# Kernel tuning notes

Hardware: AMD Instinct MI355X
Metric: run time of the kernel (lower is better)

The kernel has to match this reference:

```python
import math
import jax, jax.numpy as jnp
import numpy as np

N = 262144
DIMS_IN = 8
DIMS_C = 4
UNITS = 64
BINS = 10
N_PERMS = 3  # ceil(log2(8))
N_BLOCKS = 2 * N_PERMS
MIN_BW = 0.001
MIN_BH = 0.001
MIN_D = 0.001
EPS = 1e-6
LOG2 = float(np.log(2.0))


def build_masks():
    bits = np.array([[int(ch) for ch in np.binary_repr(i, N_PERMS)] for i in range(DIMS_IN)])
    bits = bits[:, ::-1].T  # (N_PERMS, DIMS_IN), LSB-first
    m = np.repeat(bits, 2, axis=0).astype(bool)  # repeat_interleave(2, dim=0)
    m[1::2] ^= True
    return m

MASKS = build_masks()  # (6, 8) bool, each row has 4 True


def rational_quadratic_spline(inputs, uw, uh, ud):
    # inputs: (N, D); uw/uh: (N, D, K); ud: (N, D, K+1). left=bottom=0, right=top=1.
    K = uw.shape[-1]
    widths = MIN_BW + (1.0 - MIN_BW * K) * jax.nn.softmax(uw, axis=-1)
    cw = jnp.cumsum(widths, axis=-1)
    cw = jnp.concatenate([jnp.zeros_like(cw[..., :1]), cw], axis=-1)
    cw = cw.at[..., -1].set(1.0)
    widths = cw[..., 1:] - cw[..., :-1]

    deriv = (MIN_D + jax.nn.softplus(ud)) / (MIN_D + LOG2)

    heights = MIN_BH + (1.0 - MIN_BH * K) * jax.nn.softmax(uh, axis=-1)
    ch = jnp.cumsum(heights, axis=-1)
    ch = jnp.concatenate([jnp.zeros_like(ch[..., :1]), ch], axis=-1)
    ch = ch.at[..., -1].set(1.0)
    heights = ch[..., 1:] - ch[..., :-1]

    # searchsorted on bin edges (forward uses cumwidths)
    locs = cw.at[..., -1].add(EPS)
    bin_idx = jnp.clip(jnp.sum(inputs[..., None] >= locs, axis=-1) - 1, 0, K - 1)
    g = lambda a: jnp.take_along_axis(a, bin_idx[..., None], axis=-1)[..., 0]

    in_cw = g(cw)
    in_bw = g(widths)
    in_ch = g(ch)
    delta = heights / widths
    in_delta = g(delta)
    in_d = g(deriv)
    in_dp1 = g(deriv[..., 1:])
    in_h = g(heights)

    theta = (inputs - in_cw) / in_bw
    tomt = theta * (1.0 - theta)
    numerator = in_h * (in_delta * theta ** 2 + in_d * tomt)
    denominator = in_delta + (in_d + in_dp1 - 2.0 * in_delta) * tomt
    outputs = in_ch + numerator / denominator
    deriv_num = in_delta ** 2 * (in_dp1 * theta ** 2 + 2.0 * in_delta * tomt + in_d * (1.0 - theta) ** 2)
    logabsdet = jnp.log(deriv_num) - 2.0 * jnp.log(denominator)
    return outputs, logabsdet


def unconstrained_rqs(inputs, uw, uh, ud):
    inside = jnp.all((inputs >= 0.0) & (inputs <= 1.0), axis=-1)  # (N,)
    x_in = jnp.clip(inputs, 0.0, 1.0)
    o, lad = rational_quadratic_spline(x_in, uw, uh, ud)
    outputs = jnp.where(inside[:, None], o, inputs)
    logabsdet = jnp.where(inside[:, None], lad, 0.0)
    return outputs, logabsdet


def setup_inputs() -> dict:
    key = jax.random.key(0)
    ks = jax.random.split(key, 10)
    out_dim = 4 * (3 * BINS + 1)  # every mask has 4 transformed dims
    in_dim = 4 + DIMS_C
    inp = {
        'x': jax.random.uniform(ks[0], (N, DIMS_IN), dtype=jnp.float32),
        'c': jax.random.normal(ks[1], (N, DIMS_C), dtype=jnp.float32),
        'W1': jax.random.normal(ks[2], (N_BLOCKS, in_dim, UNITS), dtype=jnp.float32) * 0.1,
        'b1': jax.random.normal(ks[3], (N_BLOCKS, UNITS), dtype=jnp.float32) * 0.1,
        'W2': jax.random.normal(ks[4], (N_BLOCKS, UNITS, UNITS), dtype=jnp.float32) * 0.1,
        'b2': jax.random.normal(ks[5], (N_BLOCKS, UNITS), dtype=jnp.float32) * 0.1,
        'W3': jax.random.normal(ks[6], (N_BLOCKS, UNITS, out_dim), dtype=jnp.float32) * 0.1,
        'b3': jax.random.normal(ks[7], (N_BLOCKS, out_dim), dtype=jnp.float32) * 0.1,
    }
    return inp


def reference(x, c, W1, b1, W2, b2, W3, b3):
    # ConditionalFlow.log_prob: forward transform, returns jac
    jac = jnp.zeros((x.shape[0],), dtype=x.dtype)
    for i in range(N_BLOCKS):
        mask = MASKS[i]
        cond_idx = np.nonzero(mask)[0]
        trafo_idx = np.nonzero(~mask)[0]
        x_cond = jnp.concatenate([x[:, cond_idx], c], axis=1)
        h = jax.nn.leaky_relu(x_cond @ W1[i] + b1[i], 0.01)
        h = jax.nn.leaky_relu(h @ W2[i] + b2[i], 0.01)
        out = (h @ W3[i] + b3[i]).reshape(x.shape[0], len(trafo_idx), 3 * BINS + 1)
        x_t = x[:, trafo_idx]
        x_out, bj = unconstrained_rqs(x_t, out[..., :BINS], out[..., BINS:2 * BINS], out[..., 2 * BINS:])
        x = x.at[:, trafo_idx].set(x_out)
        jac = jac + bj.sum(axis=1)
    return jac
```

## Files before the change

kernel.cpp:

```cpp
#include <hip/hip_runtime.h>
#include <hip/hip_bf16.h>
#include <math.h>

#define TPB 704
#define NWV 11
#define WGS 176
#define NBLK 6
#define SWA_U16 30720
#define CHUNKS 60
#define DNORM (1.0f / (0.001f + 0.69314718055994530942f))

typedef float  f32x4  __attribute__((ext_vector_type(4)));
typedef short  bf16x8 __attribute__((ext_vector_type(8)));

#define MFMA16(A, B, C) __builtin_amdgcn_mfma_f32_16x16x32_bf16((A), (B), (C), 0, 0, 0)


__device__ __forceinline__ float leaky(float a) { return a >= 0.f ? a : 0.01f * a; }

__device__ __forceinline__ unsigned int bfbits(float f) {
    unsigned int u = __float_as_uint(f);
    return (u + 0x7fffu + ((u >> 16) & 1u)) >> 16;
}

__device__ __forceinline__ unsigned int pkcvt(float a, float b) {
    __hip_bfloat162 t = __float22bfloat162_rn(make_float2(a, b));
    union { __hip_bfloat162 b2; unsigned int u; } cv;
    cv.b2 = t;
    return cv.u;
}

__global__ void prep_kernel(const float* __restrict__ W1, const float* __restrict__ B1,
                            const float* __restrict__ W2, const float* __restrict__ B2,
                            const float* __restrict__ W3, const float* __restrict__ B3,
                            unsigned short* __restrict__ wsf)
{
    const int blk = blockIdx.x;
    const int tid = threadIdx.x;
    unsigned short* baseA = wsf + blk * 5120;
    unsigned short* baseB = wsf + SWA_U16 + blk * 8192;
    const float* w1 = W1 + blk * 512;
    const float* w2 = W2 + blk * 4096;
    const float* w3 = W3 + blk * 7936;

    if (tid < 512) {
        const int tile = tid >> 7, u = (tid >> 3) & 15, i = tid & 7;
        baseA[tid] = (unsigned short)bfbits(w1[i * 64 + tile * 16 + u]);
    }
    for (int e = tid; e < 4096; e += 1024) {
        const int ks = e >> 11, tile = (e >> 9) & 3, lane = (e >> 3) & 63, i = e & 7;
        const int k = ks * 32 + (lane >> 4) * 8 + i, col = tile * 16 + (lane & 15);
        baseA[512 + e] = (unsigned short)bfbits(w2[k * 64 + col]);
    }
    for (int e = tid; e < 8192; e += 1024) {
        const int ks = e >> 12, tile = (e >> 9) & 7, lane = (e >> 3) & 63, i = e & 7;
        const int k = ks * 32 + (lane >> 4) * 8 + i, col = tile * 16 + (lane & 15);
        const float f = (col < 124) ? w3[k * 124 + col] : 0.f;
        baseB[e] = (unsigned short)bfbits(f);
    }
    float* bb = reinterpret_cast<float*>(baseA + 4608);
    if (tid < 64) { bb[tid] = B1[blk * 64 + tid]; bb[64 + tid] = B2[blk * 64 + tid]; }
    if (tid >= 128 && tid < 256) {
        const int j = tid - 128;
        bb[128 + j] = (j < 124) ? B3[blk * 124 + j] : 0.f;
    }
}

__global__ __launch_bounds__(TPB, 3) void flow_kernel(
    const float* __restrict__ X, const float* __restrict__ C4,
    const unsigned short* __restrict__ WSF, float* __restrict__ JAC, int n)
{
    __shared__ __align__(16) unsigned short s_w[SWA_U16];
    __shared__ __align__(16) unsigned char  s_u[87296];
    __shared__ __align__(16) float          s_x[1584];

    const int tid   = threadIdx.x;
    const int wv    = tid >> 6;
    const int ln    = tid & 63;
    const int col16 = ln & 15;
    const int g     = ln >> 4;
    const int srow  = wv * 16 + col16;
    const int wgBase = blockIdx.x * WGS;

    unsigned short* hh = reinterpret_cast<unsigned short*>(s_u + wv * 7936);
    float*          op = reinterpret_cast<float*>(s_u + wv * 7936);

    {
        const int s   = tid >> 2;
        const int d0  = (tid & 3) * 2;
        const int smp = wgBase + s;
        float2 xv = make_float2(0.5f, 0.5f);
        if (smp < n)
            xv = reinterpret_cast<const float2*>(X)[(size_t)smp * 4 + (tid & 3)];
        s_x[s * 9 + d0]     = xv.x;
        s_x[s * 9 + d0 + 1] = xv.y;
    }
    float4 cvv = make_float4(0.f, 0.f, 0.f, 0.f);
    if (wgBase + srow < n)
        cvv = reinterpret_cast<const float4*>(C4)[(size_t)wgBase + srow];

    {
        #pragma unroll
        for (int r = 0; r < 6; ++r) {
            const int ch = r * NWV + wv;
            if (ch < CHUNKS) {
                const int off = ch * 512;
                __builtin_amdgcn_global_load_lds(
                    (const __attribute__((address_space(1))) unsigned int*)(WSF + off + ln * 8),
                    (__attribute__((address_space(3))) unsigned int*)(&s_w[off]),
                    16, 0, 0);
            }
        }
    }
    __syncthreads();

    const int fB = g * 4;
    float jacl = 0.f;

    #pragma unroll 1
    for (int blk = 0; blk < NBLK; ++blk) {
        const int wA = blk * 5120;
        const float* biasf = reinterpret_cast<const float*>(&s_w[wA + 4608]);
        const unsigned short* w3g = WSF + SWA_U16 + blk * 8192;

        const int p  = blk >> 1;
        const int cb = (blk & 1) ^ 1;
        const int tb = blk & 1;
        const int lm = (1 << p) - 1;

        float xcf[8];
        #pragma unroll
        for (int j = 0; j < 4; ++j) {
            const int cd = ((j >> p) << (p + 1)) | (cb << p) | (j & lm);
            xcf[j] = s_x[srow * 9 + cd];
        }
        xcf[4] = cvv.x; xcf[5] = cvv.y; xcf[6] = cvv.z; xcf[7] = cvv.w;

        union { unsigned int u[4]; bf16x8 v; } bxh;
        #pragma unroll
        for (int q = 0; q < 4; ++q)
            bxh.u[q] = (g == 0) ? pkcvt(xcf[2 * q], xcf[2 * q + 1]) : 0u;

        #pragma unroll
        for (int tile = 0; tile < 4; ++tile) {
            f32x4 a1 = *reinterpret_cast<const f32x4*>(&biasf[tile * 16 + fB]);
            const bf16x8 wh = *reinterpret_cast<const bf16x8*>(&s_w[wA + tile * 128 + col16 * 8]);
            a1 = MFMA16(wh, bxh.v, a1);
            uint2 pw;
            pw.x = pkcvt(leaky(a1[0]), leaky(a1[1]));
            pw.y = pkcvt(leaky(a1[2]), leaky(a1[3]));
            *reinterpret_cast<uint2*>(&hh[col16 * 72 + tile * 16 + fB]) = pw;
        }

        f32x4 acc2[4];
        #pragma unroll
        for (int tile = 0; tile < 4; ++tile)
            acc2[tile] = *reinterpret_cast<const f32x4*>(&biasf[64 + tile * 16 + fB]);
        #pragma unroll
        for (int ks = 0; ks < 2; ++ks) {
            const bf16x8 hf = *reinterpret_cast<const bf16x8*>(&hh[col16 * 72 + ks * 32 + g * 8]);
            #pragma unroll
            for (int tile = 0; tile < 4; ++tile) {
                const bf16x8 wh = *reinterpret_cast<const bf16x8*>(
                    &s_w[wA + 512 + (ks * 4 + tile) * 512 + ln * 8]);
                acc2[tile] = MFMA16(wh, hf, acc2[tile]);
            }
        }
        #pragma unroll
        for (int tile = 0; tile < 4; ++tile) {
            uint2 pw;
            pw.x = pkcvt(leaky(acc2[tile][0]), leaky(acc2[tile][1]));
            pw.y = pkcvt(leaky(acc2[tile][2]), leaky(acc2[tile][3]));
            *reinterpret_cast<uint2*>(&hh[col16 * 72 + tile * 16 + fB]) = pw;
        }

        f32x4 acc3[8];
        #pragma unroll
        for (int tile = 0; tile < 8; ++tile)
            acc3[tile] = *reinterpret_cast<const f32x4*>(&biasf[128 + tile * 16 + fB]);
        #pragma unroll
        for (int ks = 0; ks < 2; ++ks) {
            const bf16x8 hf = *reinterpret_cast<const bf16x8*>(&hh[col16 * 72 + ks * 32 + g * 8]);
            #pragma unroll
            for (int tile = 0; tile < 8; ++tile) {
                const bf16x8 wh = *reinterpret_cast<const bf16x8*>(
                    w3g + (ks * 8 + tile) * 512 + ln * 8);
                acc3[tile] = MFMA16(wh, hf, acc3[tile]);
            }
        }

        #pragma unroll
        for (int tile = 0; tile < 8; ++tile)
            if (tile * 16 + fB < 124)
                *reinterpret_cast<f32x4*>(&op[col16 * 124 + tile * 16 + fB]) = acc3[tile];

        float xt[4];
        #pragma unroll
        for (int j = 0; j < 4; ++j) {
            const int td = ((j >> p) << (p + 1)) | (tb << p) | (j & lm);
            xt[j] = s_x[srow * 9 + td];
        }
        const float xmn = fminf(fminf(xt[0], xt[1]), fminf(xt[2], xt[3]));
        const float xmx = fmaxf(fmaxf(xt[0], xt[1]), fmaxf(xt[2], xt[3]));
        const bool inside = (xmn >= 0.f) && (xmx <= 1.f);
        float xtv = (g == 1) ? xt[1] : xt[0];
        xtv = (g == 2) ? xt[2] : xtv;
        xtv = (g == 3) ? xt[3] : xtv;
        const int ti = ((g >> p) << (p + 1)) | (tb << p) | (g & lm);

        float ov[31];
        {
            const float* ob = op + col16 * 124 + g * 31;
            #pragma unroll
            for (int j = 0; j < 31; ++j) ov[j] = ob[j];
        }

        float ew[10];
        #pragma unroll
        for (int k = 0; k < 10; ++k) ew[k] = __expf(ov[k]);
        const float sw = (((ew[0] + ew[1]) + (ew[2] + ew[3])) + ((ew[4] + ew[5]) + (ew[6] + ew[7])))
                         + (ew[8] + ew[9]);
        const float fw = 0.99f / sw;
        float Cw[11];
        Cw[0] = 0.f;
        #pragma unroll
        for (int k = 1; k <= 9; ++k) Cw[k] = Cw[k - 1] + (0.001f + ew[k - 1] * fw);
        Cw[10] = 1.0f;

        float eh[10];
        #pragma unroll
        for (int k = 0; k < 10; ++k) eh[k] = __expf(ov[10 + k]);
        const float sh = (((eh[0] + eh[1]) + (eh[2] + eh[3])) + ((eh[4] + eh[5]) + (eh[6] + eh[7])))
                         + (eh[8] + eh[9]);
        const float fh = 0.99f / sh;
        float Ch[11];
        Ch[0] = 0.f;
        #pragma unroll
        for (int k = 1; k <= 9; ++k) Ch[k] = Ch[k - 1] + (0.001f + eh[k - 1] * fh);
        Ch[10] = 1.0f;

        const float xin = fminf(fmaxf(xtv, 0.f), 1.f);
        float in_cw = 0.f, in_cwp1 = Cw[1], in_ch = 0.f, in_chp1 = Ch[1];
        float u_d = ov[20], u_dp1 = ov[21];
        #pragma unroll
        for (int k = 1; k < 10; ++k) {
            const bool ge = (xin >= Cw[k]);
            in_cw   = ge ? Cw[k]      : in_cw;
            in_cwp1 = ge ? Cw[k + 1]  : in_cwp1;
            in_ch   = ge ? Ch[k]      : in_ch;
            in_chp1 = ge ? Ch[k + 1]  : in_chp1;
            u_d     = ge ? ov[20 + k] : u_d;
            u_dp1   = ge ? ov[21 + k] : u_dp1;
        }
        const float in_bw = in_cwp1 - in_cw;
        const float in_h  = in_chp1 - in_ch;
        const float sp_d   = (u_d   > 15.f) ? u_d   : __logf(1.f + __expf(u_d));
        const float sp_dp1 = (u_dp1 > 15.f) ? u_dp1 : __logf(1.f + __expf(u_dp1));
        const float in_d   = (0.001f + sp_d)   * DNORM;
        const float in_dp1 = (0.001f + sp_dp1) * DNORM;

        const float th   = (xin - in_cw) / in_bw;
        const float tomt = th * (1.f - th);
        const float dl   = in_h / in_bw;
        const float nume = in_h * (dl * th * th + in_d * tomt);
        const float deno = dl + (in_d + in_dp1 - 2.f * dl) * tomt;
        const float xout = in_ch + nume / deno;
        const float omt  = 1.f - th;
        const float dnum = dl * dl * (in_dp1 * th * th + 2.f * dl * tomt + in_d * omt * omt);
        const float lad  = __logf(dnum) - 2.f * __logf(deno);

        jacl += inside ? lad : 0.f;
        s_x[srow * 9 + ti] = inside ? xout : xtv;
    }

    jacl += __shfl_xor(jacl, 16);
    jacl += __shfl_xor(jacl, 32);
    if (ln < 16) {
        const int smp = wgBase + wv * 16 + ln;
        if (smp < n) JAC[smp] = jacl;
    }
}

extern "C" void kernel_launch(void* const* d_in, const int* in_sizes, int n_in,
                              void* d_out, int out_size, void* d_ws, size_t ws_size,
                              hipStream_t stream) {
    (void)n_in; (void)ws_size;
    const float* X  = (const float*)d_in[0];
    const float* C4 = (const float*)d_in[1];
    const float* W1 = (const float*)d_in[2];
    const float* B1 = (const float*)d_in[3];
    const float* W2 = (const float*)d_in[4];
    const float* B2 = (const float*)d_in[5];
    const float* W3 = (const float*)d_in[6];
    const float* B3 = (const float*)d_in[7];
    float* out = (float*)d_out;
    unsigned short* wsf = (unsigned short*)d_ws;

    hipLaunchKernelGGL(prep_kernel, dim3(NBLK), dim3(1024), 0, stream,
                       W1, B1, W2, B2, W3, B3, wsf);

    const int n = in_sizes[0] / 8;
    const int grid = (n + WGS - 1) / WGS;
    hipLaunchKernelGGL(flow_kernel, dim3(grid), dim3(TPB), 0, stream,
                       X, C4, wsf, out, n);
}
```

Measured before the change: 168.3 us.

## Keep only layer-1 weights and biases in LDS, stream W2/W3 from global, widen workgroup

```diff
diff --git a/kernel.cpp b/kernel.cpp
--- a/kernel.cpp
+++ b/kernel.cpp
@@ -2,12 +2,10 @@
 #include <hip/hip_bf16.h>
 #include <math.h>
 
-#define TPB 704
-#define NWV 11
-#define WGS 176
+#define TPB 1024
+#define NWV 16
+#define WGS 256
 #define NBLK 6
-#define SWA_U16 30720
-#define CHUNKS 60
 #define DNORM (1.0f / (0.001f + 0.69314718055994530942f))
 
 typedef float  f32x4  __attribute__((ext_vector_type(4)));
@@ -37,8 +35,8 @@
 {
     const int blk = blockIdx.x;
     const int tid = threadIdx.x;
-    unsigned short* baseA = wsf + blk * 5120;
-    unsigned short* baseB = wsf + SWA_U16 + blk * 8192;
+    unsigned short* baseA = wsf + blk * 1024;
+    unsigned short* baseB = wsf + 6144 + blk * 12288;
     const float* w1 = W1 + blk * 512;
     const float* w2 = W2 + blk * 4096;
     const float* w3 = W3 + blk * 7936;
@@ -47,32 +45,34 @@
         const int tile = tid >> 7, u = (tid >> 3) & 15, i = tid & 7;
         baseA[tid] = (unsigned short)bfbits(w1[i * 64 + tile * 16 + u]);
     }
+    float* bb = reinterpret_cast<float*>(baseA + 512);
+    if (tid >= 512 && tid < 576)        bb[tid - 512]      = B1[blk * 64 + (tid - 512)];
+    else if (tid >= 576 && tid < 640)   bb[tid - 512]      = B2[blk * 64 + (tid - 576)];
+    else if (tid >= 640 && tid < 768) {
+        const int j = tid - 640;
+        bb[128 + j] = (j < 124) ? B3[blk * 124 + j] : 0.f;
+    }
+
     for (int e = tid; e < 4096; e += 1024) {
         const int ks = e >> 11, tile = (e >> 9) & 3, lane = (e >> 3) & 63, i = e & 7;
         const int k = ks * 32 + (lane >> 4) * 8 + i, col = tile * 16 + (lane & 15);
-        baseA[512 + e] = (unsigned short)bfbits(w2[k * 64 + col]);
+        baseB[e] = (unsigned short)bfbits(w2[k * 64 + col]);
     }
     for (int e = tid; e < 8192; e += 1024) {
         const int ks = e >> 12, tile = (e >> 9) & 7, lane = (e >> 3) & 63, i = e & 7;
         const int k = ks * 32 + (lane >> 4) * 8 + i, col = tile * 16 + (lane & 15);
         const float f = (col < 124) ? w3[k * 124 + col] : 0.f;
-        baseB[e] = (unsigned short)bfbits(f);
-    }
-    float* bb = reinterpret_cast<float*>(baseA + 4608);
-    if (tid < 64) { bb[tid] = B1[blk * 64 + tid]; bb[64 + tid] = B2[blk * 64 + tid]; }
-    if (tid >= 128 && tid < 256) {
-        const int j = tid - 128;
-        bb[128 + j] = (j < 124) ? B3[blk * 124 + j] : 0.f;
-    }
-}
-
-__global__ __launch_bounds__(TPB, 3) void flow_kernel(
+        baseB[4096 + e] = (unsigned short)bfbits(f);
+    }
+}
+
+__global__ __launch_bounds__(TPB, 4) void flow_kernel(
     const float* __restrict__ X, const float* __restrict__ C4,
-    const unsigned short* __restrict__ WSF, float* __restrict__ JAC, int n)
+    const unsigned short* __restrict__ WSF, float* __restrict__ JAC)
 {
-    __shared__ __align__(16) unsigned short s_w[SWA_U16];
-    __shared__ __align__(16) unsigned char  s_u[87296];
-    __shared__ __align__(16) float          s_x[1584];
+    __shared__ __align__(16) unsigned short s_w[6144];
+    __shared__ __align__(16) unsigned char  s_u[126976];
+    __shared__ __align__(16) float          s_x[2304];
 
     const int tid   = threadIdx.x;
     const int wv    = tid >> 6;
@@ -86,31 +86,20 @@
     float*          op = reinterpret_cast<float*>(s_u + wv * 7936);
 
     {
-        const int s   = tid >> 2;
-        const int d0  = (tid & 3) * 2;
-        const int smp = wgBase + s;
-        float2 xv = make_float2(0.5f, 0.5f);
-        if (smp < n)
-            xv = reinterpret_cast<const float2*>(X)[(size_t)smp * 4 + (tid & 3)];
+        const int s  = tid >> 2;
+        const int d0 = (tid & 3) * 2;
+        const float2 xv = reinterpret_cast<const float2*>(X)[(size_t)(wgBase + s) * 4 + (tid & 3)];
         s_x[s * 9 + d0]     = xv.x;
         s_x[s * 9 + d0 + 1] = xv.y;
     }
-    float4 cvv = make_float4(0.f, 0.f, 0.f, 0.f);
-    if (wgBase + srow < n)
-        cvv = reinterpret_cast<const float4*>(C4)[(size_t)wgBase + srow];
-
-    {
-        #pragma unroll
-        for (int r = 0; r < 6; ++r) {
-            const int ch = r * NWV + wv;
-            if (ch < CHUNKS) {
-                const int off = ch * 512;
-                __builtin_amdgcn_global_load_lds(
-                    (const __attribute__((address_space(1))) unsigned int*)(WSF + off + ln * 8),
-                    (__attribute__((address_space(3))) unsigned int*)(&s_w[off]),
-                    16, 0, 0);
-            }
-        }
+    const float4 cvv = reinterpret_cast<const float4*>(C4)[(size_t)wgBase + srow];
+
+    if (wv < 12) {
+        const int off = wv * 512;
+        __builtin_amdgcn_global_load_lds(
+            (const __attribute__((address_space(1))) unsigned int*)(WSF + off + ln * 8),
+            (__attribute__((address_space(3))) unsigned int*)(&s_w[off]),
+            16, 0, 0);
     }
     __syncthreads();
 
@@ -119,9 +108,9 @@
 
     #pragma unroll 1
     for (int blk = 0; blk < NBLK; ++blk) {
-        const int wA = blk * 5120;
-        const float* biasf = reinterpret_cast<const float*>(&s_w[wA + 4608]);
-        const unsigned short* w3g = WSF + SWA_U16 + blk * 8192;
+        const int wA = blk * 1024;
+        const float* biasf = reinterpret_cast<const float*>(&s_w[wA + 512]);
+        const unsigned short* wBg = WSF + 6144 + blk * 12288;
 
         const int p  = blk >> 1;
         const int cb = (blk & 1) ^ 1;
@@ -162,7 +151,7 @@
             #pragma unroll
             for (int tile = 0; tile < 4; ++tile) {
                 const bf16x8 wh = *reinterpret_cast<const bf16x8*>(
-                    &s_w[wA + 512 + (ks * 4 + tile) * 512 + ln * 8]);
+                    wBg + (ks * 4 + tile) * 512 + ln * 8);
                 acc2[tile] = MFMA16(wh, hf, acc2[tile]);
             }
         }
@@ -184,7 +173,7 @@
             #pragma unroll
             for (int tile = 0; tile < 8; ++tile) {
                 const bf16x8 wh = *reinterpret_cast<const bf16x8*>(
-                    w3g + (ks * 8 + tile) * 512 + ln * 8);
+                    wBg + 4096 + (ks * 8 + tile) * 512 + ln * 8);
                 acc3[tile] = MFMA16(wh, hf, acc3[tile]);
             }
         }
@@ -275,10 +264,8 @@
 
     jacl += __shfl_xor(jacl, 16);
     jacl += __shfl_xor(jacl, 32);
-    if (ln < 16) {
-        const int smp = wgBase + wv * 16 + ln;
-        if (smp < n) JAC[smp] = jacl;
-    }
+    if (ln < 16)
+        JAC[(size_t)wgBase + wv * 16 + ln] = jacl;
 }
 
 extern "C" void kernel_launch(void* const* d_in, const int* in_sizes, int n_in,
@@ -300,7 +287,6 @@
                        W1, B1, W2, B2, W3, B3, wsf);
 
     const int n = in_sizes[0] / 8;
-    const int grid = (n + WGS - 1) / WGS;
-    hipLaunchKernelGGL(flow_kernel, dim3(grid), dim3(TPB), 0, stream,
-                       X, C4, wsf, out, n);
-}
+    hipLaunchKernelGGL(flow_kernel, dim3(n / WGS), dim3(TPB), 0, stream,
+                       X, C4, wsf, out);
+}
```

Result: faster. 146.1 us (-13.2%).
